# Kernel tuning notes

Measured on AMD Instinct MI355X. Metric: run time of the kernel, lower is better.

The kernel has to match this reference:

```python
import jax, jax.numpy as jnp
import numpy as np

N_NODES, N_EDGES, B = 5000, 160000, 8
IN_DIM, NB, RH = 64, 8, 64
MUL0, MUL1, MUL2 = 32, 16, 8
NW = 144  # 32*3 + 16*2 + 8*2 tensor-product path weights per edge
R_MAX, AVG_NEI = 6.0, 32.0
NL, POOL_H, OUT_D = 4, 128, 512


def setup_inputs():
    ks = jax.random.split(jax.random.key(0), 24)
    f = lambda k, shape, scale=1.0: jax.random.normal(k, shape, jnp.float32) * scale
    return {
        "x": f(ks[0], (N_NODES, IN_DIM)),
        "pos": f(ks[1], (N_NODES, 3)),
        "W_in": f(ks[2], (IN_DIM, MUL0), IN_DIM ** -0.5),
        "Wr1": f(ks[3], (NL, NB, RH), NB ** -0.5), "br1": jnp.zeros((NL, RH)),
        "Wr2": f(ks[4], (NL, RH, RH), RH ** -0.5), "br2": jnp.zeros((NL, RH)),
        "Wr3": f(ks[5], (NL, RH, NW), RH ** -0.5), "br3": jnp.zeros((NL, NW)),
        "Wm0": f(ks[6], (NL, 56, MUL0), 56 ** -0.5),
        "Wm1": f(ks[7], (NL, 48, MUL1), 48 ** -0.5),
        "Wm2": f(ks[8], (NL, 40, MUL2), 40 ** -0.5),
        "Ws0": f(ks[9], (NL, MUL0, MUL0), MUL0 ** -0.5),
        "Ws1": f(ks[10], (NL, MUL1, MUL1), MUL1 ** -0.5),
        "Ws2": f(ks[11], (NL, MUL2, MUL2), MUL2 ** -0.5),
        "Wg": f(ks[12], (NL, MUL0, MUL1 + MUL2), MUL0 ** -0.5), "bg": jnp.zeros((NL, MUL1 + MUL2)),
        "Wp1": f(ks[13], (MUL0, POOL_H), MUL0 ** -0.5), "bp1": jnp.zeros((POOL_H,)),
        "Wp2": f(ks[14], (POOL_H, POOL_H), POOL_H ** -0.5), "bp2": jnp.zeros((POOL_H,)),
        "Wp3": f(ks[15], (POOL_H, 1), POOL_H ** -0.5), "bp3": jnp.zeros((1,)),
        "Wo1": f(ks[16], (MUL0, OUT_D * 2), MUL0 ** -0.5), "bo1": jnp.zeros((OUT_D * 2,)),
        "g1": jnp.ones((OUT_D * 2,)), "be1": jnp.zeros((OUT_D * 2,)),
        "Wo2": f(ks[17], (OUT_D * 2, OUT_D), (OUT_D * 2) ** -0.5), "bo2": jnp.zeros((OUT_D,)),
        "g2": jnp.ones((OUT_D,)), "be2": jnp.zeros((OUT_D,)),
        "edge_index": jax.random.randint(ks[18], (2, N_EDGES), 0, N_NODES),
        "batch": jnp.sort(jax.random.randint(ks[19], (N_NODES,), 0, B)),
    }


def _ln(x, gamma, beta):
    m = x.mean(-1, keepdims=True)
    v = x.var(-1, keepdims=True)
    return (x - m) / jnp.sqrt(v + 1e-5) * gamma + beta


def _forward(x, pos, W_in, Wr1, br1, Wr2, br2, Wr3, br3, Wm0, Wm1, Wm2,
             Ws0, Ws1, Ws2, Wg, bg, Wp1, bp1, Wp2, bp2, Wp3, bp3,
             Wo1, bo1, g1, be1, Wo2, bo2, g2, be2, edge_index, batch):
    N = x.shape[0]
    src, dst = edge_index[0], edge_index[1]
    vec = pos[src] - pos[dst]                       # [E,3]
    r = jnp.sqrt(jnp.sum(vec * vec, -1) + 1e-12)    # [E]
    u = vec / r[:, None]
    # Bessel radial basis with smooth polynomial cutoff (p=6)
    nfreq = jnp.arange(1, NB + 1, dtype=x.dtype)
    bess = jnp.sqrt(2.0 / R_MAX) * jnp.sin(nfreq * jnp.pi * r[:, None] / R_MAX) / r[:, None]
    t = jnp.clip(r / R_MAX, 0.0, 1.0)
    fcut = (1.0 - 28.0 * t**6 + 48.0 * t**7 - 21.0 * t**8) * (r < R_MAX).astype(x.dtype)
    edge_emb = bess * fcut[:, None]                 # [E,NB]
    # real spherical harmonics of edge direction, component normalization
    ux, uy, uz = u[:, 0], u[:, 1], u[:, 2]
    Y1 = jnp.sqrt(3.0) * u                          # [E,3]
    Y2 = jnp.stack([15.0**0.5 * ux * uy, 15.0**0.5 * uy * uz,
                    0.5 * 5.0**0.5 * (3.0 * uz * uz - 1.0),
                    15.0**0.5 * ux * uz, 0.5 * 15.0**0.5 * (ux * ux - uy * uy)], -1)  # [E,5]
    # input embedding: 64x0e -> hidden irreps (only scalar path exists; l>0 start at 0)
    s = x @ W_in                                    # [N,32]
    v = jnp.zeros((N, MUL1, 3), x.dtype)            # [N,16,3] 1o
    q = jnp.zeros((N, MUL2, 5), x.dtype)            # [N,8,5]  2e
    for i in range(NL):
        w = jax.nn.silu(edge_emb @ Wr1[i] + br1[i])
        w = jax.nn.silu(w @ Wr2[i] + br2[i])
        w = w @ Wr3[i] + br3[i]                     # [E,144] per-edge TP path weights
        w_ss, w_sv, w_sq, w_vs, w_vv, w_qs, w_qq = jnp.split(w, [32, 64, 96, 112, 128, 136], -1)
        se, ve, qe = s[src], v[src], q[src]         # gather
        # tensor-product messages, grouped by output irrep
        m0 = jnp.concatenate([w_ss * se,
                              w_vv * jnp.einsum('ecm,em->ec', ve, Y1) / 3.0**0.5,
                              w_qq * jnp.einsum('ecm,em->ec', qe, Y2) / 5.0**0.5], -1)   # [E,56]
        m1 = jnp.concatenate([(w_sv * se)[:, :, None] * Y1[:, None, :],
                              w_vs[:, :, None] * ve], 1)                                  # [E,48,3]
        m2 = jnp.concatenate([(w_sq * se)[:, :, None] * Y2[:, None, :],
                              w_qs[:, :, None] * qe], 1)                                  # [E,40,5]
        a0 = jax.ops.segment_sum(m0, dst, num_segments=N) / AVG_NEI
        a1 = jax.ops.segment_sum(m1, dst, num_segments=N) / AVG_NEI
        a2 = jax.ops.segment_sum(m2, dst, num_segments=N) / AVG_NEI
        # per-irrep linear mix + self-connection
        ns = a0 @ Wm0[i] + s @ Ws0[i]
        nv = jnp.einsum('ncm,co->nom', a1, Wm1[i]) + jnp.einsum('ncm,co->nom', v, Ws1[i])
        nq = jnp.einsum('ncm,co->nom', a2, Wm2[i]) + jnp.einsum('ncm,co->nom', q, Ws2[i])
        # gate activation + resnet
        gates = jax.nn.sigmoid(ns @ Wg[i] + bg[i])  # [N,24]
        s = s + jax.nn.silu(ns)
        v = v + nv * gates[:, :MUL1, None]
        q = q + nq * gates[:, MUL1:, None]
    # attention pooling over scalar channels (scatter-softmax per graph)
    logits = (jax.nn.silu(jax.nn.silu(s @ Wp1 + bp1) @ Wp2 + bp2) @ Wp3 + bp3)[:, 0]
    mx = jax.ops.segment_max(logits, batch, num_segments=B)
    z = jnp.exp(logits - mx[batch])
    att = z / jax.ops.segment_sum(z, batch, num_segments=B)[batch]
    gpool = jax.ops.segment_sum(s * att[:, None], batch, num_segments=B)  # [B,32]
    h = jax.nn.silu(_ln(gpool @ Wo1 + bo1, g1, be1))
    return _ln(h @ Wo2 + bo2, g2, be2)              # [B,512]


def reference(x, pos, W_in, Wr1, br1, Wr2, br2, Wr3, br3, Wm0, Wm1, Wm2,
              Ws0, Ws1, Ws2, Wg, bg, Wp1, bp1, Wp2, bp2, Wp3, bp3,
              Wo1, bo1, g1, be1, Wo2, bo2, g2, be2, edge_index, batch):
    return _forward(x, pos, W_in, Wr1, br1, Wr2, br2, Wr3, br3, Wm0, Wm1, Wm2,
                    Ws0, Ws1, Ws2, Wg, bg, Wp1, bp1, Wp2, bp2, Wp3, bp3,
                    Wo1, bo1, g1, be1, Wo2, bo2, g2, be2, edge_index, batch)
```

## Files before the change

### kernel.cpp

```cpp
#include <hip/hip_runtime.h>

constexpr int NN  = 5000;
constexpr int NE  = 160000;
constexpr int NB_ = 8;
constexpr float RMAX   = 6.0f;
constexpr float INV_AVG = 1.0f/32.0f;
constexpr float SQ3  = 1.7320508075688772f;
constexpr float ISQ3 = 0.5773502691896258f;
constexpr float ISQ5 = 0.4472135954999579f;
constexpr float SQ15 = 3.872983346207417f;
constexpr float SQ5  = 2.2360679774997896f;
constexpr float PIF  = 3.14159265358979323846f;

__device__ __forceinline__ float sigmoid_f(float x){
    return 1.0f / (1.0f + __expf(-x));
}
__device__ __forceinline__ float silu_f(float x){ return x * sigmoid_f(x); }

__global__ void k_geom(const float* __restrict__ pos, const int* __restrict__ ei,
                       float* __restrict__ geom, int* __restrict__ counts){
    int e = blockIdx.x*256 + threadIdx.x;
    if (e >= NE) return;
    int s = ei[e], d = ei[NE + e];
    float vx = pos[3*s]-pos[3*d], vy = pos[3*s+1]-pos[3*d+1], vz = pos[3*s+2]-pos[3*d+2];
    float r2 = vx*vx + vy*vy + vz*vz + 1e-12f;
    float r  = sqrtf(r2);
    float ir = 1.0f/r;
    float ux = vx*ir, uy = vy*ir, uz = vz*ir;
    float t  = fminf(r*(1.0f/RMAX), 1.0f);
    float t2=t*t, t3=t2*t, t6=t3*t3, t7=t6*t, t8=t7*t;
    float fc = (1.0f - 28.0f*t6 + 48.0f*t7 - 21.0f*t8) * (r < RMAX ? 1.0f : 0.0f);
    float cb = sqrtf(2.0f/RMAX) * ir * fc;
    float w[16];
    #pragma unroll
    for (int k=0;k<8;k++){
        float arg = (float)(k+1) * (PIF/RMAX) * r;
        w[k] = cb * sinf(arg);
    }
    w[8]  = SQ3*ux; w[9] = SQ3*uy; w[10] = SQ3*uz;
    w[11] = SQ15*ux*uy; w[12] = SQ15*uy*uz; w[13] = 0.5f*SQ5*(3.0f*uz*uz-1.0f);
    w[14] = SQ15*ux*uz; w[15] = 0.5f*SQ15*(ux*ux-uy*uy);
    float4* o = (float4*)(geom + (size_t)e*16);
    o[0] = make_float4(w[0],w[1],w[2],w[3]);
    o[1] = make_float4(w[4],w[5],w[6],w[7]);
    o[2] = make_float4(w[8],w[9],w[10],w[11]);
    o[3] = make_float4(w[12],w[13],w[14],w[15]);
    atomicAdd(&counts[d], 1);
}

__global__ void k_scan(int* __restrict__ cr, int* __restrict__ fpos){
    __shared__ int part[256];
    int t = threadIdx.x;
    const int CH = (NN + 255)/256;
    int base = t*CH;
    int s = 0;
    for (int i=0;i<CH;i++){ int idx = base+i; if (idx < NN) s += cr[idx]; }
    part[t] = s; __syncthreads();
    for (int off=1; off<256; off<<=1){
        int v = (t >= off) ? part[t-off] : 0;
        __syncthreads();
        part[t] += v;
        __syncthreads();
    }
    int run = (t==0) ? 0 : part[t-1];
    for (int i=0;i<CH;i++){
        int idx = base+i;
        if (idx < NN){
            int c = cr[idx];
            cr[idx]  = run;
            fpos[idx] = run;
            run += c;
        } else if (idx == NN){
            cr[idx] = run;
        }
    }
}

__global__ void k_fill(const int* __restrict__ ei, int* __restrict__ fpos,
                       int* __restrict__ elist, int* __restrict__ slot){
    int e = blockIdx.x*256 + threadIdx.x;
    if (e >= NE) return;
    int d = ei[NE+e];
    int p = atomicAdd(&fpos[d], 1);
    elist[p] = e;
    slot[e]  = p;
}

__global__ void k_sinit(const float* __restrict__ x, const float* __restrict__ Win,
                        float* __restrict__ sA){
    int tid = blockIdx.x*256 + threadIdx.x;
    int n = tid >> 5, o = tid & 31;
    if (n >= NN) return;
    float a = 0.f;
    #pragma unroll
    for (int k=0;k<64;k++) a = fmaf(x[n*64+k], Win[k*32+o], a);
    sA[n*32+o] = a;
}

__launch_bounds__(256, 4)
__global__ void k_mlp(const float* __restrict__ geom, const int* __restrict__ slot,
                      const float* __restrict__ Wr1, const float* __restrict__ br1,
                      const float* __restrict__ Wr2, const float* __restrict__ br2,
                      const float* __restrict__ Wr3, const float* __restrict__ br3,
                      float* __restrict__ wbuf, int layer){
    __shared__ __align__(16) float w1s[8*64];
    __shared__ __align__(16) float w2s[64*64];
    __shared__ __align__(16) float b1s[64], b2s[64];
    __shared__ __align__(16) float b3s[144];
    __shared__ __align__(16) float embs[64][8];
    __shared__ __align__(16) float hs[64][68];
    __shared__ int   slots[64];

    const int t  = threadIdx.x;
    const int e0 = blockIdx.x * 64;
    const float* W1 = Wr1 + layer*(8*64);
    const float* b1 = br1 + layer*64;
    const float* W2 = Wr2 + layer*(64*64);
    const float* b2 = br2 + layer*64;
    const float* W3 = Wr3 + layer*(64*144);
    const float* b3 = br3 + layer*144;

    {
        const float4* W2v = (const float4*)W2;
        float4* w2v = (float4*)w2s;
        #pragma unroll
        for (int i=0;i<4;i++) w2v[t + 256*i] = W2v[t + 256*i];
        if (t < 128) ((float4*)w1s)[t] = ((const float4*)W1)[t];
        if (t < 64){ b1s[t] = b1[t]; b2s[t] = b2[t]; slots[t] = slot[e0 + t]; }
        if (t < 144) b3s[t] = b3[t];
        if (t < 128){
            ((float4*)embs)[t] = *((const float4*)geom + (size_t)(e0 + (t>>1))*4 + (t&1));
        }
    }
    __syncthreads();

    const int eg = t >> 3;
    const int jg = t & 7;
    const int ea = eg*2, eb = ea+1;

    float a0[2][8];
    #pragma unroll
    for (int i=0;i<2;i++)
        #pragma unroll
        for (int u=0;u<8;u++) a0[i][u] = b1s[8*jg+u];
    #pragma unroll
    for (int k=0;k<8;k++){
        float e_a = embs[ea][k], e_b = embs[eb][k];
        #pragma unroll
        for (int u=0;u<8;u++){
            float wv = w1s[k*64 + 8*jg + u];
            a0[0][u] = fmaf(e_a, wv, a0[0][u]);
            a0[1][u] = fmaf(e_b, wv, a0[1][u]);
        }
    }
    #pragma unroll
    for (int i=0;i<2;i++){
        int e = ea + i;
        float4 p0 = make_float4(silu_f(a0[i][0]), silu_f(a0[i][1]), silu_f(a0[i][2]), silu_f(a0[i][3]));
        float4 p1 = make_float4(silu_f(a0[i][4]), silu_f(a0[i][5]), silu_f(a0[i][6]), silu_f(a0[i][7]));
        *(float4*)&hs[e][8*jg]     = p0;
        *(float4*)&hs[e][8*jg + 4] = p1;
    }
    __syncthreads();

    float a1[2][8];
    #pragma unroll
    for (int i=0;i<2;i++)
        #pragma unroll
        for (int u=0;u<8;u++) a1[i][u] = b2s[8*jg+u];
    #pragma unroll
    for (int k=0;k<64;k++){
        float h_a = hs[ea][k], h_b = hs[eb][k];
        float4 wA = *(const float4*)&w2s[k*64 + 8*jg];
        float4 wB = *(const float4*)&w2s[k*64 + 8*jg + 4];
        a1[0][0]=fmaf(h_a,wA.x,a1[0][0]); a1[0][1]=fmaf(h_a,wA.y,a1[0][1]);
        a1[0][2]=fmaf(h_a,wA.z,a1[0][2]); a1[0][3]=fmaf(h_a,wA.w,a1[0][3]);
        a1[0][4]=fmaf(h_a,wB.x,a1[0][4]); a1[0][5]=fmaf(h_a,wB.y,a1[0][5]);
        a1[0][6]=fmaf(h_a,wB.z,a1[0][6]); a1[0][7]=fmaf(h_a,wB.w,a1[0][7]);
        a1[1][0]=fmaf(h_b,wA.x,a1[1][0]); a1[1][1]=fmaf(h_b,wA.y,a1[1][1]);
        a1[1][2]=fmaf(h_b,wA.z,a1[1][2]); a1[1][3]=fmaf(h_b,wA.w,a1[1][3]);
        a1[1][4]=fmaf(h_b,wB.x,a1[1][4]); a1[1][5]=fmaf(h_b,wB.y,a1[1][5]);
        a1[1][6]=fmaf(h_b,wB.z,a1[1][6]); a1[1][7]=fmaf(h_b,wB.w,a1[1][7]);
    }
    __syncthreads();
    #pragma unroll
    for (int i=0;i<2;i++){
        int e = ea + i;
        float4 p0 = make_float4(silu_f(a1[i][0]), silu_f(a1[i][1]), silu_f(a1[i][2]), silu_f(a1[i][3]));
        float4 p1 = make_float4(silu_f(a1[i][4]), silu_f(a1[i][5]), silu_f(a1[i][6]), silu_f(a1[i][7]));
        *(float4*)&hs[e][8*jg]     = p0;
        *(float4*)&hs[e][8*jg + 4] = p1;
    }
    __syncthreads();

    float c2[2][18];
    #pragma unroll
    for (int i=0;i<2;i++)
        #pragma unroll
        for (int u=0;u<18;u++) c2[i][u] = b3s[18*jg+u];

    float* w3c = w2s;
    for (int ch=0; ch<4; ++ch){
        const float4* src = (const float4*)(W3 + 16*ch*144);
        float4* dst = (float4*)w3c;
        dst[t]       = src[t];
        dst[t+256]   = src[t+256];
        if (t < 64) dst[t+512] = src[t+512];
        __syncthreads();
        #pragma unroll
        for (int kk=0;kk<16;kk++){
            int k = 16*ch + kk;
            float h_a = hs[ea][k], h_b = hs[eb][k];
            #pragma unroll
            for (int u2=0;u2<9;u2++){
                float2 wv = *(const float2*)&w3c[kk*144 + 18*jg + 2*u2];
                c2[0][2*u2]   = fmaf(h_a, wv.x, c2[0][2*u2]);
                c2[0][2*u2+1] = fmaf(h_a, wv.y, c2[0][2*u2+1]);
                c2[1][2*u2]   = fmaf(h_b, wv.x, c2[1][2*u2]);
                c2[1][2*u2+1] = fmaf(h_b, wv.y, c2[1][2*u2+1]);
            }
        }
        __syncthreads();
    }
    #pragma unroll
    for (int i=0;i<2;i++){
        float* wo = wbuf + (size_t)slots[ea+i]*144 + 18*jg;
        #pragma unroll
        for (int u2=0;u2<9;u2++)
            *(float2*)(wo + 2*u2) = make_float2(c2[i][2*u2], c2[i][2*u2+1]);
    }
}

__launch_bounds__(256, 8)
__global__ void k_gather(const int* __restrict__ rowp, const int* __restrict__ elist,
                         const int* __restrict__ ei, const float* __restrict__ geom,
                         const float* __restrict__ wbuf,
                         const float* __restrict__ s_in, const float* __restrict__ v_in,
                         const float* __restrict__ q_in,
                         float* __restrict__ s_out, float* __restrict__ v_out,
                         float* __restrict__ q_out,
                         const float* __restrict__ Wm0, const float* __restrict__ Wm1,
                         const float* __restrict__ Wm2,
                         const float* __restrict__ Ws0, const float* __restrict__ Ws1,
                         const float* __restrict__ Ws2,
                         const float* __restrict__ Wg, const float* __restrict__ bg,
                         int layer){
    __shared__ float pacc[4][400];
    __shared__ float lacc[400];
    __shared__ float lns[32];
    __shared__ float lgate[24];
    const int n = blockIdx.x;
    const int t = threadIdx.x;
    const int w = t >> 6;
    const int lane = t & 63;

    int s0_w, s0_o, s0_ob;
    if (lane < 32){ s0_w = lane;            s0_o = lane;          s0_ob = lane; }
    else if (lane < 48){ s0_w = 112+(lane-32); s0_o = 3*(lane-32); s0_ob = lane; }
    else if (lane < 56){ s0_w = 136+(lane-48); s0_o = 5*(lane-48); s0_ob = lane; }
    else { int R = lane-56; s0_w = 32+R; s0_o = R; s0_ob = 56+3*R; }
    int s1_w, s1_o, s1_ob;
    if (lane < 24){ int R = lane+8; s1_w = 32+R; s1_o = R;     s1_ob = 56+3*R; }
    else if (lane < 40){ int j = lane-24; s1_w = 96+j; s1_o = 3*j; s1_ob = 152+3*j; }
    else { int R = lane-40; s1_w = 64+R; s1_o = R; s1_ob = 200+5*R; }
    int s2_w, s2_o, s2_ob;
    if (lane < 8){ int R = lane+24; s2_w = 64+R; s2_o = R;   s2_ob = 200+5*R; }
    else { int j = lane-8; s2_w = 128+j; s2_o = 5*j; s2_ob = 360+5*j; }

    float a0[3] = {0.f,0.f,0.f};
    float a1[5] = {0.f,0.f,0.f,0.f,0.f};
    float a2[5] = {0.f,0.f,0.f,0.f,0.f};

    const int beg = rowp[n], end = rowp[n+1];
    for (int idx = beg + w; idx < end; idx += 4){
        int e   = elist[idx];
        int src = ei[e];
        const float* gp = geom + (size_t)e*16;
        float4 y14 = *(const float4*)(gp + 8);
        float4 y58 = *(const float4*)(gp + 12);
        const float* wp = wbuf + (size_t)idx*144;
        const float* sp = s_in + (size_t)src*32;
        const float* vp = v_in + (size_t)src*48;
        const float* qp = q_in + (size_t)src*40;
        {
            float wv = wp[s0_w];
            if (lane < 32){
                a0[0] = fmaf(wv, sp[s0_o], a0[0]);
            } else if (lane < 48){
                float dv = vp[s0_o]*y14.x + vp[s0_o+1]*y14.y + vp[s0_o+2]*y14.z;
                a0[0] = fmaf(wv*ISQ3, dv, a0[0]);
            } else if (lane < 56){
                float dq = qp[s0_o]*y14.w + qp[s0_o+1]*y58.x + qp[s0_o+2]*y58.y
                         + qp[s0_o+3]*y58.z + qp[s0_o+4]*y58.w;
                a0[0] = fmaf(wv*ISQ5, dq, a0[0]);
            } else {
                float tmp = wv * sp[s0_o];
                a0[0] = fmaf(tmp, y14.x, a0[0]);
                a0[1] = fmaf(tmp, y14.y, a0[1]);
                a0[2] = fmaf(tmp, y14.z, a0[2]);
            }
        }
        {
            float wv = wp[s1_w];
            if (lane < 24){
                float tmp = wv * sp[s1_o];
                a1[0] = fmaf(tmp, y14.x, a1[0]);
                a1[1] = fmaf(tmp, y14.y, a1[1]);
                a1[2] = fmaf(tmp, y14.z, a1[2]);
            } else if (lane < 40){
                a1[0] = fmaf(wv, vp[s1_o],   a1[0]);
                a1[1] = fmaf(wv, vp[s1_o+1], a1[1]);
                a1[2] = fmaf(wv, vp[s1_o+2], a1[2]);
            } else {
                float tmp = wv * sp[s1_o];
                a1[0] = fmaf(tmp, y14.w, a1[0]);
                a1[1] = fmaf(tmp, y58.x, a1[1]);
                a1[2] = fmaf(tmp, y58.y, a1[2]);
                a1[3] = fmaf(tmp, y58.z, a1[3]);
                a1[4] = fmaf(tmp, y58.w, a1[4]);
            }
        }
        if (lane < 16){
            float wv = wp[s2_w];
            if (lane < 8){
                float tmp = wv * sp[s2_o];
                a2[0] = fmaf(tmp, y14.w, a2[0]);
                a2[1] = fmaf(tmp, y58.x, a2[1]);
                a2[2] = fmaf(tmp, y58.y, a2[2]);
                a2[3] = fmaf(tmp, y58.z, a2[3]);
                a2[4] = fmaf(tmp, y58.w, a2[4]);
            } else {
                a2[0] = fmaf(wv, qp[s2_o],   a2[0]);
                a2[1] = fmaf(wv, qp[s2_o+1], a2[1]);
                a2[2] = fmaf(wv, qp[s2_o+2], a2[2]);
                a2[3] = fmaf(wv, qp[s2_o+3], a2[3]);
                a2[4] = fmaf(wv, qp[s2_o+4], a2[4]);
            }
        }
    }
    pacc[w][s0_ob] = a0[0];
    if (lane >= 56){ pacc[w][s0_ob+1] = a0[1]; pacc[w][s0_ob+2] = a0[2]; }
    pacc[w][s1_ob] = a1[0]; pacc[w][s1_ob+1] = a1[1]; pacc[w][s1_ob+2] = a1[2];
    if (lane >= 40){ pacc[w][s1_ob+3] = a1[3]; pacc[w][s1_ob+4] = a1[4]; }
    if (lane < 16){
        #pragma unroll
        for (int u=0;u<5;u++) pacc[w][s2_ob+u] = a2[u];
    }
    __syncthreads();
    for (int c=t; c<400; c+=256)
        lacc[c] = (pacc[0][c]+pacc[1][c]+pacc[2][c]+pacc[3][c]) * INV_AVG;
    __syncthreads();

    const float* Wm0p = Wm0 + layer*(56*32);
    const float* Ws0p = Ws0 + layer*(32*32);
    const float* Wm1p = Wm1 + layer*(48*16);
    const float* Ws1p = Ws1 + layer*(16*16);
    const float* Wm2p = Wm2 + layer*(40*8);
    const float* Ws2p = Ws2 + layer*(8*8);
    const float* Wgp  = Wg  + layer*(32*24);
    const float* bgp  = bg  + layer*24;

    float nvv = 0.f, nqv = 0.f;
    if (t < 32){
        float a = 0.f;
        #pragma unroll
        for (int c=0;c<56;c++) a = fmaf(lacc[c], Wm0p[c*32+t], a);
        #pragma unroll
        for (int c=0;c<32;c++) a = fmaf(s_in[n*32+c], Ws0p[c*32+t], a);
        lns[t] = a;
    } else if (t >= 64 && t < 112){
        int o = t-64, o3 = o/3, m3 = o-3*o3;
        #pragma unroll
        for (int c=0;c<48;c++) nvv = fmaf(lacc[56+c*3+m3], Wm1p[c*16+o3], nvv);
        #pragma unroll
        for (int c=0;c<16;c++) nvv = fmaf(v_in[n*48+c*3+m3], Ws1p[c*16+o3], nvv);
    } else if (t >= 128 && t < 168){
        int o = t-128, o5 = o/5, m5 = o-5*o5;
        #pragma unroll
        for (int c=0;c<40;c++) nqv = fmaf(lacc[200+c*5+m5], Wm2p[c*8+o5], nqv);
        #pragma unroll
        for (int c=0;c<8;c++)  nqv = fmaf(q_in[n*40+c*5+m5], Ws2p[c*8+o5], nqv);
    }
    __syncthreads();
    if (t < 24){
        float a = bgp[t];
        #pragma unroll
        for (int c=0;c<32;c++) a = fmaf(lns[c], Wgp[c*24+t], a);
        lgate[t] = sigmoid_f(a);
    }
    __syncthreads();
    if (t < 32){
        s_out[n*32+t] = s_in[n*32+t] + silu_f(lns[t]);
    } else if (t >= 64 && t < 112){
        int o = t-64;
        v_out[n*48+o] = v_in[n*48+o] + nvv * lgate[o/3];
    } else if (t >= 128 && t < 168){
        int o = t-128;
        q_out[n*40+o] = q_in[n*40+o] + nqv * lgate[16+o/5];
    }
}

__launch_bounds__(128)
__global__ void k_pool(const float* __restrict__ s_in,
                       const float* __restrict__ Wp1, const float* __restrict__ bp1,
                       const float* __restrict__ Wp2, const float* __restrict__ bp2,
                       const float* __restrict__ Wp3, const float* __restrict__ bp3,
                       float* __restrict__ logits){
    __shared__ float ls[32];
    __shared__ float lh[128];
    __shared__ float wred[2];
    int n = blockIdx.x, t = threadIdx.x;
    if (t < 32) ls[t] = s_in[n*32+t];
    __syncthreads();
    float a = bp1[t];
    #pragma unroll
    for (int c=0;c<32;c++) a = fmaf(ls[c], Wp1[c*128+t], a);
    lh[t] = silu_f(a);
    __syncthreads();
    float b = bp2[t];
    #pragma unroll
    for (int k=0;k<128;k++) b = fmaf(lh[k], Wp2[k*128+t], b);
    float p = silu_f(b) * Wp3[t];
    #pragma unroll
    for (int off=32; off>0; off>>=1) p += __shfl_down(p, off, 64);
    if ((t & 63) == 0) wred[t>>6] = p;
    __syncthreads();
    if (t == 0) logits[n] = wred[0] + wred[1] + bp3[0];
}

__global__ void k_ranges(const int* __restrict__ batch, int* __restrict__ rs, int* __restrict__ re){
    int n = blockIdx.x*256 + threadIdx.x;
    if (n >= NN) return;
    int b = batch[n];
    if (n == 0 || batch[n-1] != b) rs[b] = n;
    if (n == NN-1 || batch[n+1] != b) re[b] = n+1;
}

__launch_bounds__(1024)
__global__ void k_bmax(const float* __restrict__ logits, const int* __restrict__ rs,
                       const int* __restrict__ re, float* __restrict__ mx){
    __shared__ float red[1024];
    int b = blockIdx.x, t = threadIdx.x;
    int lo = rs[b], hi = re[b];
    float m = -3.0e38f;
    for (int n=lo+t; n<hi; n+=1024) m = fmaxf(m, logits[n]);
    red[t] = m; __syncthreads();
    for (int s2=512; s2>0; s2>>=1){ if (t<s2) red[t] = fmaxf(red[t], red[t+s2]); __syncthreads(); }
    if (t==0) mx[b] = red[0];
}

__global__ void k_z(const float* __restrict__ logits, const int* __restrict__ batch,
                    const float* __restrict__ mx, float* __restrict__ zbuf,
                    float* __restrict__ denom){
    int n = blockIdx.x*256 + threadIdx.x;
    if (n >= NN) return;
    int b = batch[n];
    float z = __expf(logits[n] - mx[b]);
    zbuf[n] = z;
    atomicAdd(&denom[b], z);
}

__launch_bounds__(1024)
__global__ void k_gpool(const float* __restrict__ s_in, const float* __restrict__ zbuf,
                        const int* __restrict__ rs, const int* __restrict__ re,
                        const float* __restrict__ denom, float* __restrict__ gpool){
    __shared__ float red[32][32];
    int b = blockIdx.x, t = threadIdx.x;
    int c = t & 31, g = t >> 5;
    int lo = rs[b], hi = re[b];
    float a = 0.f;
    for (int n=lo+g; n<hi; n+=32) a = fmaf(zbuf[n], s_in[n*32+c], a);
    red[g][c] = a; __syncthreads();
    if (t < 32){
        float s2 = 0.f;
        #pragma unroll
        for (int g2=0; g2<32; g2++) s2 += red[g2][t];
        gpool[b*32+t] = s2 / denom[b];
    }
}

__launch_bounds__(1024)
__global__ void k_out1(const float* __restrict__ gpool, const float* __restrict__ Wo1,
                       const float* __restrict__ bo1, const float* __restrict__ g1,
                       const float* __restrict__ be1, float* __restrict__ hbuf){
    __shared__ float lg[32];
    __shared__ float red[1024];
    __shared__ float stats[2];
    int b = blockIdx.x, t = threadIdx.x;
    if (t < 32) lg[t] = gpool[b*32+t];
    __syncthreads();
    float a = bo1[t];
    #pragma unroll
    for (int c=0;c<32;c++) a = fmaf(lg[c], Wo1[c*1024+t], a);
    red[t] = a; __syncthreads();
    for (int s2=512; s2>0; s2>>=1){ if (t<s2) red[t]+=red[t+s2]; __syncthreads(); }
    if (t==0) stats[0] = red[0]*(1.0f/1024.0f);
    __syncthreads();
    float mean = stats[0];
    float d = a - mean;
    red[t] = d*d; __syncthreads();
    for (int s2=512; s2>0; s2>>=1){ if (t<s2) red[t]+=red[t+s2]; __syncthreads(); }
    if (t==0) stats[1] = red[0]*(1.0f/1024.0f);
    __syncthreads();
    float rstd = rsqrtf(stats[1] + 1e-5f);
    hbuf[b*1024+t] = silu_f(d*rstd*g1[t] + be1[t]);
}

__launch_bounds__(1024)
__global__ void k_out2(const float* __restrict__ hbuf, const float* __restrict__ Wo2,
                       const float* __restrict__ bo2, const float* __restrict__ g2,
                       const float* __restrict__ be2, float* __restrict__ out){
    __shared__ float lh[1024];
    __shared__ float part[1024];
    __shared__ float red[1024];
    __shared__ float stats[2];
    int b = blockIdx.x, t = threadIdx.x;
    lh[t] = hbuf[b*1024 + t];
    __syncthreads();
    int j = t & 511, half = t >> 9;
    float a = (half == 0) ? bo2[j] : 0.0f;
    int k0 = half*512;
    #pragma unroll 8
    for (int k=0;k<512;k++) a = fmaf(lh[k0+k], Wo2[(size_t)(k0+k)*512 + j], a);
    part[t] = a; __syncthreads();
    float y = 0.f;
    if (t < 512) y = part[t] + part[t+512];
    red[t] = (t < 512) ? y : 0.f; __syncthreads();
    for (int s2=512; s2>0; s2>>=1){ if (t<s2) red[t]+=red[t+s2]; __syncthreads(); }
    if (t==0) stats[0] = red[0]*(1.0f/512.0f);
    __syncthreads();
    float mean = stats[0];
    float d = y - mean;
    red[t] = (t < 512) ? d*d : 0.f; __syncthreads();
    for (int s2=512; s2>0; s2>>=1){ if (t<s2) red[t]+=red[t+s2]; __syncthreads(); }
    if (t==0) stats[1] = red[0]*(1.0f/512.0f);
    __syncthreads();
    float rstd = rsqrtf(stats[1] + 1e-5f);
    if (t < 512) out[b*512+t] = d*rstd*g2[t] + be2[t];
}

extern "C" void kernel_launch(void* const* d_in, const int* in_sizes, int n_in,
                              void* d_out, int out_size, void* d_ws, size_t ws_size,
                              hipStream_t stream){
    const float* x   = (const float*)d_in[0];
    const float* pos = (const float*)d_in[1];
    const float* Win = (const float*)d_in[2];
    const float* Wr1 = (const float*)d_in[3];
    const float* br1 = (const float*)d_in[4];
    const float* Wr2 = (const float*)d_in[5];
    const float* br2 = (const float*)d_in[6];
    const float* Wr3 = (const float*)d_in[7];
    const float* br3 = (const float*)d_in[8];
    const float* Wm0 = (const float*)d_in[9];
    const float* Wm1 = (const float*)d_in[10];
    const float* Wm2 = (const float*)d_in[11];
    const float* Ws0 = (const float*)d_in[12];
    const float* Ws1 = (const float*)d_in[13];
    const float* Ws2 = (const float*)d_in[14];
    const float* Wg  = (const float*)d_in[15];
    const float* bg  = (const float*)d_in[16];
    const float* Wp1 = (const float*)d_in[17];
    const float* bp1 = (const float*)d_in[18];
    const float* Wp2 = (const float*)d_in[19];
    const float* bp2 = (const float*)d_in[20];
    const float* Wp3 = (const float*)d_in[21];
    const float* bp3 = (const float*)d_in[22];
    const float* Wo1 = (const float*)d_in[23];
    const float* bo1 = (const float*)d_in[24];
    const float* g1  = (const float*)d_in[25];
    const float* be1 = (const float*)d_in[26];
    const float* Wo2 = (const float*)d_in[27];
    const float* bo2 = (const float*)d_in[28];
    const float* g2  = (const float*)d_in[29];
    const float* be2 = (const float*)d_in[30];
    const int* ei    = (const int*)d_in[31];
    const int* batch = (const int*)d_in[32];
    float* out = (float*)d_out;

    char* wsb = (char*)d_ws;
    size_t off = 0;
    auto take = [&](size_t bytes)->char*{
        char* p = wsb + off;
        off = (off + bytes + 255) & ~(size_t)255;
        return p;
    };
    float* geom  = (float*)take((size_t)NE*16*4);
    float* wbuf  = (float*)take((size_t)NE*144*4);
    int*   rowp  = (int*)take((size_t)(NN+1)*4);
    int*   fpos  = (int*)take((size_t)NN*4);
    int*   elist = (int*)take((size_t)NE*4);
    int*   slot  = (int*)take((size_t)NE*4);
    float* sA = (float*)take((size_t)NN*32*4);
    float* sB = (float*)take((size_t)NN*32*4);
    float* vA = (float*)take((size_t)NN*48*4);
    float* vB = (float*)take((size_t)NN*48*4);
    float* qA = (float*)take((size_t)NN*40*4);
    float* qB = (float*)take((size_t)NN*40*4);
    float* logits = (float*)take((size_t)NN*4);
    float* zbuf   = (float*)take((size_t)NN*4);
    float* mx     = (float*)take(64);
    float* denom  = (float*)take(64);
    int*   rs     = (int*)take(64);
    int*   re     = (int*)take(64);
    float* gpool  = (float*)take((size_t)NB_*32*4);
    float* hbuf   = (float*)take((size_t)NB_*1024*4);
    (void)ws_size; (void)in_sizes; (void)n_in; (void)out_size;

    hipMemsetAsync(rowp, 0, (size_t)(NN+1)*4, stream);
    hipMemsetAsync(vA,   0, (size_t)NN*48*4, stream);
    hipMemsetAsync(qA,   0, (size_t)NN*40*4, stream);
    hipMemsetAsync(denom,0, 64, stream);
    hipMemsetAsync(rs,   0, 64, stream);
    hipMemsetAsync(re,   0, 64, stream);

    k_geom<<<(NE+255)/256, 256, 0, stream>>>(pos, ei, geom, rowp);
    k_scan<<<1, 256, 0, stream>>>(rowp, fpos);
    k_fill<<<(NE+255)/256, 256, 0, stream>>>(ei, fpos, elist, slot);
    k_sinit<<<(NN*32+255)/256, 256, 0, stream>>>(x, Win, sA);
    k_ranges<<<(NN+255)/256, 256, 0, stream>>>(batch, rs, re);

    float* si=sA; float* so=sB; float* vi=vA; float* vo=vB; float* qi=qA; float* qo=qB;
    for (int layer=0; layer<4; ++layer){
        k_mlp<<<NE/64, 256, 0, stream>>>(geom, slot, Wr1, br1, Wr2, br2, Wr3, br3, wbuf, layer);
        k_gather<<<NN, 256, 0, stream>>>(rowp, elist, ei, geom, wbuf, si, vi, qi, so, vo, qo,
                                         Wm0, Wm1, Wm2, Ws0, Ws1, Ws2, Wg, bg, layer);
        float* ts=si; si=so; so=ts;
        float* tv=vi; vi=vo; vo=tv;
        float* tq=qi; qi=qo; qo=tq;
    }
    k_pool<<<NN, 128, 0, stream>>>(si, Wp1, bp1, Wp2, bp2, Wp3, bp3, logits);
    k_bmax<<<NB_, 1024, 0, stream>>>(logits, rs, re, mx);
    k_z<<<(NN+255)/256, 256, 0, stream>>>(logits, batch, mx, zbuf, denom);
    k_gpool<<<NB_, 1024, 0, stream>>>(si, zbuf, rs, re, denom, gpool);
    k_out1<<<NB_, 1024, 0, stream>>>(gpool, Wo1, bo1, g1, be1, hbuf);
    k_out2<<<NB_, 1024, 0, stream>>>(hbuf, Wo2, bo2, g2, be2, out);
}
```

Baseline: 1.095 ms.

## Widen gather blocks to 8 waves and fuse softmax pooling kernels

k_gather now launches 512 threads (8 waves) per node, each wave handling every eighth edge with a two-way unrolled loop, and the partial sums are reduced across 8 shared buffers. The three pooling kernels (segment max, exp/denominator with atomics, weighted sum) become one per-graph kernel that computes max, exp, weighted sum and denominator in a single block. Memsets are merged by placing vA and qA next to each other, and rs and re share one allocation. The aim is more parallelism per node, given only about 32 edges each, and fewer launches and atomics, at the cost of more idle waves on low-degree nodes and larger shared memory.

```diff
diff --git a/kernel.cpp b/kernel.cpp
--- a/kernel.cpp
+++ b/kernel.cpp
@@ -231,7 +231,7 @@
     }
 }
 
-__launch_bounds__(256, 8)
+__launch_bounds__(512, 4)
 __global__ void k_gather(const int* __restrict__ rowp, const int* __restrict__ elist,
                          const int* __restrict__ ei, const float* __restrict__ geom,
                          const float* __restrict__ wbuf,
@@ -245,7 +245,7 @@
                          const float* __restrict__ Ws2,
                          const float* __restrict__ Wg, const float* __restrict__ bg,
                          int layer){
-    __shared__ float pacc[4][400];
+    __shared__ float pacc[8][400];
     __shared__ float lacc[400];
     __shared__ float lns[32];
     __shared__ float lgate[24];
@@ -271,8 +271,7 @@
     float a1[5] = {0.f,0.f,0.f,0.f,0.f};
     float a2[5] = {0.f,0.f,0.f,0.f,0.f};
 
-    const int beg = rowp[n], end = rowp[n+1];
-    for (int idx = beg + w; idx < end; idx += 4){
+    auto body = [&](int idx){
         int e   = elist[idx];
         int src = ei[e];
         const float* gp = geom + (size_t)e*16;
@@ -337,7 +336,16 @@
                 a2[4] = fmaf(wv, qp[s2_o+4], a2[4]);
             }
         }
-    }
+    };
+
+    const int beg = rowp[n], end = rowp[n+1];
+    int idx = beg + w;
+    for (; idx + 8 < end; idx += 16){
+        body(idx);
+        body(idx + 8);
+    }
+    if (idx < end) body(idx);
+
     pacc[w][s0_ob] = a0[0];
     if (lane >= 56){ pacc[w][s0_ob+1] = a0[1]; pacc[w][s0_ob+2] = a0[2]; }
     pacc[w][s1_ob] = a1[0]; pacc[w][s1_ob+1] = a1[1]; pacc[w][s1_ob+2] = a1[2];
@@ -347,8 +355,12 @@
         for (int u=0;u<5;u++) pacc[w][s2_ob+u] = a2[u];
     }
     __syncthreads();
-    for (int c=t; c<400; c+=256)
-        lacc[c] = (pacc[0][c]+pacc[1][c]+pacc[2][c]+pacc[3][c]) * INV_AVG;
+    for (int c=t; c<400; c+=512){
+        float s8 = 0.f;
+        #pragma unroll
+        for (int g=0; g<8; g++) s8 += pacc[g][c];
+        lacc[c] = s8 * INV_AVG;
+    }
     __syncthreads();
 
     const float* Wm0p = Wm0 + layer*(56*32);
@@ -437,45 +449,37 @@
 }
 
 __launch_bounds__(1024)
-__global__ void k_bmax(const float* __restrict__ logits, const int* __restrict__ rs,
-                       const int* __restrict__ re, float* __restrict__ mx){
+__global__ void k_spool(const float* __restrict__ logits, const float* __restrict__ s_in,
+                        const int* __restrict__ rs, const int* __restrict__ re,
+                        float* __restrict__ gpool){
     __shared__ float red[1024];
+    __shared__ float racc[32*33];
+    __shared__ float dred[32];
+    __shared__ float smx;
     int b = blockIdx.x, t = threadIdx.x;
     int lo = rs[b], hi = re[b];
     float m = -3.0e38f;
-    for (int n=lo+t; n<hi; n+=1024) m = fmaxf(m, logits[n]);
+    for (int n = lo + t; n < hi; n += 1024) m = fmaxf(m, logits[n]);
     red[t] = m; __syncthreads();
     for (int s2=512; s2>0; s2>>=1){ if (t<s2) red[t] = fmaxf(red[t], red[t+s2]); __syncthreads(); }
-    if (t==0) mx[b] = red[0];
-}
-
-__global__ void k_z(const float* __restrict__ logits, const int* __restrict__ batch,
-                    const float* __restrict__ mx, float* __restrict__ zbuf,
-                    float* __restrict__ denom){
-    int n = blockIdx.x*256 + threadIdx.x;
-    if (n >= NN) return;
-    int b = batch[n];
-    float z = __expf(logits[n] - mx[b]);
-    zbuf[n] = z;
-    atomicAdd(&denom[b], z);
-}
-
-__launch_bounds__(1024)
-__global__ void k_gpool(const float* __restrict__ s_in, const float* __restrict__ zbuf,
-                        const int* __restrict__ rs, const int* __restrict__ re,
-                        const float* __restrict__ denom, float* __restrict__ gpool){
-    __shared__ float red[32][32];
-    int b = blockIdx.x, t = threadIdx.x;
-    int c = t & 31, g = t >> 5;
-    int lo = rs[b], hi = re[b];
-    float a = 0.f;
-    for (int n=lo+g; n<hi; n+=32) a = fmaf(zbuf[n], s_in[n*32+c], a);
-    red[g][c] = a; __syncthreads();
+    if (t==0) smx = red[0];
+    __syncthreads();
+    float mx = smx;
+    int g = t >> 5, c = t & 31;
+    float acc = 0.f, zs = 0.f;
+    for (int n = lo + g; n < hi; n += 32){
+        float z = __expf(logits[n] - mx);
+        acc = fmaf(z, s_in[n*32+c], acc);
+        zs += z;
+    }
+    racc[g*33+c] = acc;
+    if (c == 0) dred[g] = zs;
+    __syncthreads();
     if (t < 32){
-        float s2 = 0.f;
-        #pragma unroll
-        for (int g2=0; g2<32; g2++) s2 += red[g2][t];
-        gpool[b*32+t] = s2 / denom[b];
+        float a = 0.f, d = 0.f;
+        #pragma unroll
+        for (int g2=0; g2<32; g2++){ a += racc[g2*33+t]; d += dred[g2]; }
+        gpool[b*32+t] = a / d;
     }
 }
 
@@ -590,28 +594,22 @@
     int*   fpos  = (int*)take((size_t)NN*4);
     int*   elist = (int*)take((size_t)NE*4);
     int*   slot  = (int*)take((size_t)NE*4);
+    float* vA = (float*)take((size_t)NN*48*4);
+    float* qA = (float*)take((size_t)NN*40*4);
     float* sA = (float*)take((size_t)NN*32*4);
     float* sB = (float*)take((size_t)NN*32*4);
-    float* vA = (float*)take((size_t)NN*48*4);
     float* vB = (float*)take((size_t)NN*48*4);
-    float* qA = (float*)take((size_t)NN*40*4);
     float* qB = (float*)take((size_t)NN*40*4);
     float* logits = (float*)take((size_t)NN*4);
-    float* zbuf   = (float*)take((size_t)NN*4);
-    float* mx     = (float*)take(64);
-    float* denom  = (float*)take(64);
     int*   rs     = (int*)take(64);
-    int*   re     = (int*)take(64);
+    int*   re     = rs + 8;
     float* gpool  = (float*)take((size_t)NB_*32*4);
     float* hbuf   = (float*)take((size_t)NB_*1024*4);
     (void)ws_size; (void)in_sizes; (void)n_in; (void)out_size;
 
     hipMemsetAsync(rowp, 0, (size_t)(NN+1)*4, stream);
-    hipMemsetAsync(vA,   0, (size_t)NN*48*4, stream);
-    hipMemsetAsync(qA,   0, (size_t)NN*40*4, stream);
-    hipMemsetAsync(denom,0, 64, stream);
+    hipMemsetAsync(vA,   0, (size_t)NN*48*4 + (size_t)NN*40*4, stream);
     hipMemsetAsync(rs,   0, 64, stream);
-    hipMemsetAsync(re,   0, 64, stream);
 
     k_geom<<<(NE+255)/256, 256, 0, stream>>>(pos, ei, geom, rowp);
     k_scan<<<1, 256, 0, stream>>>(rowp, fpos);
@@ -622,16 +620,14 @@
     float* si=sA; float* so=sB; float* vi=vA; float* vo=vB; float* qi=qA; float* qo=qB;
     for (int layer=0; layer<4; ++layer){
         k_mlp<<<NE/64, 256, 0, stream>>>(geom, slot, Wr1, br1, Wr2, br2, Wr3, br3, wbuf, layer);
-        k_gather<<<NN, 256, 0, stream>>>(rowp, elist, ei, geom, wbuf, si, vi, qi, so, vo, qo,
+        k_gather<<<NN, 512, 0, stream>>>(rowp, elist, ei, geom, wbuf, si, vi, qi, so, vo, qo,
                                          Wm0, Wm1, Wm2, Ws0, Ws1, Ws2, Wg, bg, layer);
         float* ts=si; si=so; so=ts;
         float* tv=vi; vi=vo; vo=tv;
         float* tq=qi; qi=qo; qo=tq;
     }
     k_pool<<<NN, 128, 0, stream>>>(si, Wp1, bp1, Wp2, bp2, Wp3, bp3, logits);
-    k_bmax<<<NB_, 1024, 0, stream>>>(logits, rs, re, mx);
-    k_z<<<(NN+255)/256, 256, 0, stream>>>(logits, batch, mx, zbuf, denom);
-    k_gpool<<<NB_, 1024, 0, stream>>>(si, zbuf, rs, re, denom, gpool);
+    k_spool<<<NB_, 1024, 0, stream>>>(logits, si, rs, re, gpool);
     k_out1<<<NB_, 1024, 0, stream>>>(gpool, Wo1, bo1, g1, be1, hbuf);
     k_out2<<<NB_, 1024, 0, stream>>>(hbuf, Wo2, bo2, g2, be2, out);
 }
```

Measured after the change: 1.097 ms. About the same (+0.1%).
